# Kernel tuning notes

Hardware: AMD Instinct MI355X
Metric: run time of the kernel (lower is better)

## Reference

```python
import jax, jax.numpy as jnp
import numpy as np

B, IN, OUT, GD, TD, H, W, L = 16, 512, 256, 256, 256, 32, 32, 32
EPS_BN = 1e-5


def _conv2d(x, w, pad):
    return jax.lax.conv_general_dilated(
        x, w, window_strides=(1, 1), padding=[(pad, pad), (pad, pad)],
        dimension_numbers=("NCHW", "OIHW", "NCHW"))


def _up2(x):
    return jnp.repeat(jnp.repeat(x, 2, axis=2), 2, axis=3)


def _l2n(v):  # F.normalize(p=2, dim=1), eps=1e-12
    n = jnp.sqrt(jnp.sum(v * v, axis=1, keepdims=True))
    return v / jnp.maximum(n, 1e-12)


def _context(img_embs, words_embs, mask):
    i = _l2n(img_embs)            # [B, TD, P]
    wd = _l2n(words_embs)         # [B, TD, L]
    sim = jnp.einsum("bcp,bcl->bpl", i, wd)
    sim = jnp.where(mask[:, None, :], -jnp.inf, sim)
    attn = jax.nn.softmax(sim, axis=-1)
    return jnp.einsum("bpl,bcl->bcp", attn, wd)  # [B, TD, P]


def _bn(x, w, b):  # training-mode BatchNorm2d, biased variance
    m = jnp.mean(x, axis=(0, 2, 3), keepdims=True)
    v = jnp.var(x, axis=(0, 2, 3), keepdims=True)
    return (x - m) * jax.lax.rsqrt(v + EPS_BN) * w[None, :, None, None] + b[None, :, None, None]


def setup_inputs():
    key = jax.random.key(0)
    ks = jax.random.split(key, 16)
    s = 0.02
    COND = GD + TD
    return {
        "x": jax.random.normal(ks[0], (B, IN, H, W), jnp.float32),
        "global_cond": jax.random.normal(ks[1], (B, GD), jnp.float32),
        "words_embs": jax.random.normal(ks[2], (B, TD, L), jnp.float32),
        "mask": jax.random.randint(ks[3], (B, L), 0, 2).astype(bool),
        "w_img1": jax.random.normal(ks[4], (TD, IN), jnp.float32) * s,
        "w_img2": jax.random.normal(ks[5], (TD, OUT), jnp.float32) * s,
        "w_c1": jax.random.normal(ks[6], (OUT, IN, 3, 3), jnp.float32) * s,
        "w_c2": jax.random.normal(ks[7], (OUT, OUT, 3, 3), jnp.float32) * s,
        "bn1_w": jnp.ones((IN,), jnp.float32),
        "bn1_b": jnp.zeros((IN,), jnp.float32),
        "bn2_w": jnp.ones((OUT,), jnp.float32),
        "bn2_b": jnp.zeros((OUT,), jnp.float32),
        "w_g1": jax.random.normal(ks[8], (IN, COND), jnp.float32) * s,
        "b_g1": jnp.zeros((IN,), jnp.float32),
        "w_b1": jax.random.normal(ks[9], (IN, COND), jnp.float32) * s,
        "b_b1": jnp.zeros((IN,), jnp.float32),
        "w_g2": jax.random.normal(ks[10], (OUT, COND), jnp.float32) * s,
        "b_g2": jnp.zeros((OUT,), jnp.float32),
        "w_b2": jax.random.normal(ks[11], (OUT, COND), jnp.float32) * s,
        "b_b2": jnp.zeros((OUT,), jnp.float32),
        "w_sc": jax.random.normal(ks[12], (OUT, IN, 1, 1), jnp.float32) * s,
        "b_sc": jnp.zeros((OUT,), jnp.float32),
    }


def reference(x, global_cond, words_embs, mask,
              w_img1, w_img2, w_c1, w_c2,
              bn1_w, bn1_b, bn2_w, bn2_b,
              w_g1, b_g1, w_b1, b_b1,
              w_g2, b_g2, w_b2, b_b2,
              w_sc, b_sc):
    # ---- residual path, stage 1 ----
    img1 = jnp.einsum("tc,bcp->btp", w_img1, x.reshape(B, IN, H * W))
    ctx1 = _context(img1, words_embs, mask)                 # [B, TD, H*W]
    gc = jnp.broadcast_to(global_cond[:, :, None], (B, GD, H * W))
    cond1 = jnp.concatenate([gc, ctx1], axis=1)             # [B, GD+TD, H*W]
    gamma1 = jnp.einsum("oc,bcp->bop", w_g1, cond1) + b_g1[None, :, None]
    beta1 = jnp.einsum("oc,bcp->bop", w_b1, cond1) + b_b1[None, :, None]
    out = gamma1.reshape(B, IN, H, W) * _bn(x, bn1_w, bn1_b) + beta1.reshape(B, IN, H, W)
    out = jax.nn.relu(out)
    out = _up2(out)                                         # [B, IN, 2H, 2W]
    out = _conv2d(out, w_c1, 1)                             # [B, OUT, 2H, 2W]
    h2, w2 = 2 * H, 2 * W
    # ---- residual path, stage 2 ----
    img2 = jnp.einsum("tc,bcp->btp", w_img2, out.reshape(B, OUT, h2 * w2))
    ctx2 = _context(img2, words_embs, mask)                 # [B, TD, h2*w2]
    gc2 = jnp.broadcast_to(global_cond[:, :, None], (B, GD, h2 * w2))
    cond2 = jnp.concatenate([gc2, ctx2], axis=1)
    gamma2 = jnp.einsum("oc,bcp->bop", w_g2, cond2) + b_g2[None, :, None]
    beta2 = jnp.einsum("oc,bcp->bop", w_b2, cond2) + b_b2[None, :, None]
    out = gamma2.reshape(B, OUT, h2, w2) * _bn(out, bn2_w, bn2_b) + beta2.reshape(B, OUT, h2, w2)
    out = jax.nn.relu(out)
    out = _conv2d(out, w_c2, 1)
    # ---- shortcut ----
    sc = _conv2d(_up2(x), w_sc, 0) + b_sc[None, :, None, None]
    return out + sc
```

## Files before the change

### kernel.cpp

```cpp
#include <hip/hip_runtime.h>
#include <hip/hip_bf16.h>
#include <math.h>

#define NB 16
#define CIN1 512
#define COUT 256
#define GD 256
#define TD 256
#define LL 32
#define P1 1024
#define P2 4096
#define CONDC 512

typedef __attribute__((ext_vector_type(8))) short bf16x8;
typedef __attribute__((ext_vector_type(4))) float f32x4;
typedef unsigned short u16;

__device__ __forceinline__ u16 f2b(float f) {
  __hip_bfloat16 h = __float2bfloat16(f);
  return *(u16*)&h;
}
__device__ __forceinline__ float b2f(u16 v) {
  unsigned u = ((unsigned)v) << 16;
  float f;
  __builtin_memcpy(&f, &u, 4);
  return f;
}

__global__ void bn_stats_x_kernel(const float* __restrict__ x, float* __restrict__ mean,
                                  float* __restrict__ rstd, u16* __restrict__ xbf,
                                  int C, int HW) {
  int c = blockIdx.x, t = threadIdx.x;
  float s = 0.f, sq = 0.f;
  for (int b = 0; b < NB; ++b) {
    size_t base = ((size_t)b * C + c) * HW;
    for (int i = t; i < HW; i += 256) {
      float v = x[base + i];
      s += v; sq += v * v;
      xbf[base + i] = f2b(v);
    }
  }
  __shared__ float ss[256], sq2[256];
  ss[t] = s; sq2[t] = sq; __syncthreads();
  for (int o = 128; o > 0; o >>= 1) {
    if (t < o) { ss[t] += ss[t + o]; sq2[t] += sq2[t + o]; }
    __syncthreads();
  }
  if (t == 0) {
    float n = (float)NB * (float)HW;
    float m = ss[0] / n;
    float v = sq2[0] / n - m * m;
    mean[c] = m;
    rstd[c] = rsqrtf(v + 1e-5f);
  }
}

__global__ void bn_fin_kernel(const float* __restrict__ part, float* __restrict__ mean,
                              float* __restrict__ rstd) {
  int c = threadIdx.x;
  float s = 0.f, sq = 0.f;
  const float* ps = part + (size_t)c * 256;
  const float* pq = part + 65536 + (size_t)c * 256;
  for (int i = 0; i < 256; ++i) { s += ps[i]; sq += pq[i]; }
  float n = 16.f * 4096.f;
  float m = s / n;
  mean[c] = m;
  rstd[c] = rsqrtf(sq / n - m * m + 1e-5f);
}

__global__ void wdn_kernel(const float* __restrict__ we, float* __restrict__ wdn) {
  int b = blockIdx.x >> 5, l = blockIdx.x & 31;
  int t = threadIdx.x;
  const float* base = we + (size_t)b * TD * LL + l;
  float v[4]; float sq = 0.f;
#pragma unroll
  for (int k = 0; k < 4; ++k) { v[k] = base[(size_t)(t * 4 + k) * LL]; sq += v[k] * v[k]; }
#pragma unroll
  for (int o = 32; o > 0; o >>= 1) sq += __shfl_xor(sq, o);
  float r = 1.f / fmaxf(sqrtf(sq), 1e-12f);
  float* ob = wdn + (size_t)b * TD * LL + l;
#pragma unroll
  for (int k = 0; k < 4; ++k) ob[(size_t)(t * 4 + k) * LL] = v[k] * r;
}

__global__ __launch_bounds__(256) void attnctx_kernel(
    const u16* __restrict__ img, const float* __restrict__ wdn,
    const int* __restrict__ mask, u16* __restrict__ ctx, int P) {
  __shared__ u16 imgT[2][64 * 72];
  __shared__ u16 wdnT[32 * 264];
  __shared__ u16 wdnC[256 * 40];
  __shared__ u16 attnB[64 * 40];
  __shared__ float sqP[4][64];
  __shared__ float rnL[64];
  const int b = blockIdx.y, p0 = blockIdx.x * 64;
  const int tid = threadIdx.x;
  const int w = tid >> 6, lane = tid & 63;
  const int l15 = lane & 15, lg = lane >> 4;
  const u16* ib = img + (size_t)b * TD * P;
  const float* wb = wdn + (size_t)b * TD * LL;

  for (int i = tid; i < TD * LL; i += 256) {
    int t = i >> 5, l = i & 31;
    u16 v = f2b(wb[i]);
    wdnT[l * 264 + t] = v;
    wdnC[t * 40 + l] = v;
  }

  f32x4 s0 = {}, s1 = {};
  float ssq = 0.f;
  unsigned pk[8];
#pragma unroll
  for (int i = 0; i < 8; ++i) {
    int t = w * 16 + 2 * i;
    u16 h0 = ib[(size_t)t * P + p0 + lane];
    u16 h1 = ib[(size_t)(t + 1) * P + p0 + lane];
    float v0 = b2f(h0), v1 = b2f(h1);
    ssq += v0 * v0 + v1 * v1;
    pk[i] = (unsigned)h0 | ((unsigned)h1 << 16);
  }
#pragma unroll
  for (int i = 0; i < 8; ++i)
    *(unsigned*)(imgT[0] + lane * 72 + w * 16 + 2 * i) = pk[i];
  __syncthreads();

  for (int q = 0; q < 4; ++q) {
    const int cur = q & 1;
    if (q < 3) {
#pragma unroll
      for (int i = 0; i < 8; ++i) {
        int t = (q + 1) * 64 + w * 16 + 2 * i;
        u16 h0 = ib[(size_t)t * P + p0 + lane];
        u16 h1 = ib[(size_t)(t + 1) * P + p0 + lane];
        float v0 = b2f(h0), v1 = b2f(h1);
        ssq += v0 * v0 + v1 * v1;
        pk[i] = (unsigned)h0 | ((unsigned)h1 << 16);
      }
    }
#pragma unroll
    for (int ks = 0; ks < 2; ++ks) {
      bf16x8 a = *(const bf16x8*)(imgT[cur] + (w * 16 + l15) * 72 + ks * 32 + lg * 8);
      bf16x8 b0 = *(const bf16x8*)(wdnT + l15 * 264 + q * 64 + ks * 32 + lg * 8);
      bf16x8 b1 = *(const bf16x8*)(wdnT + (16 + l15) * 264 + q * 64 + ks * 32 + lg * 8);
      s0 = __builtin_amdgcn_mfma_f32_16x16x32_bf16(a, b0, s0, 0, 0, 0);
      s1 = __builtin_amdgcn_mfma_f32_16x16x32_bf16(a, b1, s1, 0, 0, 0);
    }
    if (q < 3) {
#pragma unroll
      for (int i = 0; i < 8; ++i)
        *(unsigned*)(imgT[cur ^ 1] + lane * 72 + w * 16 + 2 * i) = pk[i];
      __syncthreads();
    }
  }
  sqP[w][lane] = ssq;
  __syncthreads();
  if (tid < 64) {
    float s = sqP[0][tid] + sqP[1][tid] + sqP[2][tid] + sqP[3][tid];
    rnL[tid] = 1.f / fmaxf(sqrtf(s), 1e-12f);
  }
  __syncthreads();
  const bool m0 = mask[b * LL + l15] != 0;
  const bool m1 = mask[b * LL + 16 + l15] != 0;
#pragma unroll
  for (int k = 0; k < 4; ++k) {
    float rn = rnL[w * 16 + lg * 4 + k];
    float v0 = m0 ? -INFINITY : s0[k] * rn;
    float v1 = m1 ? -INFINITY : s1[k] * rn;
    float mx = fmaxf(v0, v1);
#pragma unroll
    for (int o = 1; o < 16; o <<= 1) mx = fmaxf(mx, __shfl_xor(mx, o));
    float e0 = expf(v0 - mx), e1 = expf(v1 - mx);
    float sm = e0 + e1;
#pragma unroll
    for (int o = 1; o < 16; o <<= 1) sm += __shfl_xor(sm, o);
    float inv = 1.f / sm;
    int px = w * 16 + lg * 4 + k;
    attnB[px * 40 + l15] = f2b(e0 * inv);
    attnB[px * 40 + 16 + l15] = f2b(e1 * inv);
  }
  __syncthreads();
  f32x4 acc[4][4] = {};
  bf16x8 bfr[4];
#pragma unroll
  for (int pt = 0; pt < 4; ++pt)
    bfr[pt] = *(const bf16x8*)(attnB + (pt * 16 + l15) * 40 + lg * 8);
#pragma unroll
  for (int cc = 0; cc < 4; ++cc) {
    bf16x8 a = *(const bf16x8*)(wdnC + ((w * 4 + cc) * 16 + l15) * 40 + lg * 8);
#pragma unroll
    for (int pt = 0; pt < 4; ++pt)
      acc[cc][pt] = __builtin_amdgcn_mfma_f32_16x16x32_bf16(a, bfr[pt], acc[cc][pt], 0, 0, 0);
  }
#pragma unroll
  for (int cc = 0; cc < 4; ++cc) {
#pragma unroll
    for (int pt = 0; pt < 4; ++pt) {
#pragma unroll
      for (int k = 0; k < 4; ++k) {
        int c = (w * 4 + cc) * 16 + lg * 4 + k;
        ctx[((size_t)b * TD + c) * P + p0 + pt * 16 + l15] = f2b(acc[cc][pt][k]);
      }
    }
  }
}

__global__ __launch_bounds__(256) void attnimg_kernel(
    const u16* __restrict__ W2p, const u16* __restrict__ xin,
    const float* __restrict__ wdn, const int* __restrict__ mask,
    u16* __restrict__ ctx, int P) {
  __shared__ u16 smem[(33792 + 16896) / 2];
  __shared__ float rnL[64];
  u16* imgT  = smem;
  u16* Xl    = smem + 16896;
  u16* wdnT  = smem + 16896;
  u16* wdnC  = smem;
  u16* attnB = smem + 10240;
  const int b = blockIdx.y, p0 = blockIdx.x * 64;
  const int tid = threadIdx.x;
  const int w = tid >> 6, lane = tid & 63;
  const int l15 = lane & 15, lg = lane >> 4;
  const u16* xb = xin + (size_t)b * COUT * P;
  const float* wb = wdn + (size_t)b * TD * LL;

  const int xr = tid >> 3, xcG = tid & 7;
  const int csw = xr ^ (((xcG >> 1) & 3) << 3);
  const u16* xsrc = xb + (size_t)xr * P + p0 + xcG * 8;
  u16 xst[8];
  {
    union { u16 u[8]; uint4 q; } xu;
    xu.q = *(const uint4*)xsrc;
#pragma unroll
    for (int i = 0; i < 8; ++i) xst[i] = xu.u[i];
  }
#pragma unroll
  for (int i = 0; i < 8; ++i)
    Xl[(xcG * 8 + i) * 40 + csw] = xst[i];
  __syncthreads();

  f32x4 acc[16];
#pragma unroll
  for (int tt = 0; tt < 16; ++tt) acc[tt] = (f32x4){0.f, 0.f, 0.f, 0.f};
  for (int c0b = 0; c0b < 8; ++c0b) {
    const int cur = c0b & 1;
    if (c0b + 1 < 8) {
      union { u16 u[8]; uint4 q; } xu;
      xu.q = *(const uint4*)(xsrc + (size_t)((c0b + 1) * 32) * P);
#pragma unroll
      for (int i = 0; i < 8; ++i) xst[i] = xu.u[i];
    }
    bf16x8 aA = *(const bf16x8*)(Xl + cur * 2560 + (w * 16 + l15) * 40 + ((lg ^ w) << 3));
#pragma unroll
    for (int tt = 0; tt < 16; ++tt) {
      bf16x8 bfr = *(const bf16x8*)(W2p + (((size_t)c0b * 16 + tt) * 64 + lane) * 8);
      acc[tt] = __builtin_amdgcn_mfma_f32_16x16x32_bf16(aA, bfr, acc[tt], 0, 0, 0);
    }
    if (c0b + 1 < 8) {
      const int nxt = cur ^ 1;
#pragma unroll
      for (int i = 0; i < 8; ++i)
        Xl[nxt * 2560 + (xcG * 8 + i) * 40 + csw] = xst[i];
      __syncthreads();
    }
  }
#pragma unroll
  for (int k = 0; k < 4; ++k) {
    float s = 0.f;
#pragma unroll
    for (int tt = 0; tt < 16; ++tt) s += acc[tt][k] * acc[tt][k];
#pragma unroll
    for (int o = 1; o < 16; o <<= 1) s += __shfl_xor(s, o);
    if (l15 == 0) rnL[w * 16 + lg * 4 + k] = 1.f / fmaxf(sqrtf(s), 1e-12f);
  }
#pragma unroll
  for (int tt = 0; tt < 16; ++tt)
#pragma unroll
    for (int k = 0; k < 4; ++k)
      imgT[(w * 16 + lg * 4 + k) * 264 + tt * 16 + l15] = f2b(acc[tt][k]);
  __syncthreads();

  for (int i = tid; i < TD * LL; i += 256) {
    int t = i >> 5, l = i & 31;
    wdnT[l * 264 + t] = f2b(wb[i]);
  }
  __syncthreads();
  f32x4 s0 = {}, s1 = {};
#pragma unroll
  for (int q = 0; q < 4; ++q) {
#pragma unroll
    for (int ks = 0; ks < 2; ++ks) {
      bf16x8 a = *(const bf16x8*)(imgT + (w * 16 + l15) * 264 + q * 64 + ks * 32 + lg * 8);
      bf16x8 b0 = *(const bf16x8*)(wdnT + l15 * 264 + q * 64 + ks * 32 + lg * 8);
      bf16x8 b1 = *(const bf16x8*)(wdnT + (16 + l15) * 264 + q * 64 + ks * 32 + lg * 8);
      s0 = __builtin_amdgcn_mfma_f32_16x16x32_bf16(a, b0, s0, 0, 0, 0);
      s1 = __builtin_amdgcn_mfma_f32_16x16x32_bf16(a, b1, s1, 0, 0, 0);
    }
  }
  const bool m0 = mask[b * LL + l15] != 0;
  const bool m1 = mask[b * LL + 16 + l15] != 0;
  float a0[4], a1[4];
#pragma unroll
  for (int k = 0; k < 4; ++k) {
    float rn = rnL[w * 16 + lg * 4 + k];
    float v0 = m0 ? -INFINITY : s0[k] * rn;
    float v1 = m1 ? -INFINITY : s1[k] * rn;
    float mx = fmaxf(v0, v1);
#pragma unroll
    for (int o = 1; o < 16; o <<= 1) mx = fmaxf(mx, __shfl_xor(mx, o));
    float e0 = expf(v0 - mx), e1 = expf(v1 - mx);
    float sm = e0 + e1;
#pragma unroll
    for (int o = 1; o < 16; o <<= 1) sm += __shfl_xor(sm, o);
    float inv = 1.f / sm;
    a0[k] = e0 * inv; a1[k] = e1 * inv;
  }
  __syncthreads();

  for (int i = tid; i < TD * LL; i += 256) {
    int t = i >> 5, l = i & 31;
    wdnC[t * 40 + l] = f2b(wb[i]);
  }
#pragma unroll
  for (int k = 0; k < 4; ++k) {
    int px = w * 16 + lg * 4 + k;
    attnB[px * 40 + l15] = f2b(a0[k]);
    attnB[px * 40 + 16 + l15] = f2b(a1[k]);
  }
  __syncthreads();
  f32x4 acc2[4][4] = {};
  bf16x8 bfr[4];
#pragma unroll
  for (int pt = 0; pt < 4; ++pt)
    bfr[pt] = *(const bf16x8*)(attnB + (pt * 16 + l15) * 40 + lg * 8);
#pragma unroll
  for (int cc = 0; cc < 4; ++cc) {
    bf16x8 a = *(const bf16x8*)(wdnC + ((w * 4 + cc) * 16 + l15) * 40 + lg * 8);
#pragma unroll
    for (int pt = 0; pt < 4; ++pt)
      acc2[cc][pt] = __builtin_amdgcn_mfma_f32_16x16x32_bf16(a, bfr[pt], acc2[cc][pt], 0, 0, 0);
  }
#pragma unroll
  for (int cc = 0; cc < 4; ++cc) {
#pragma unroll
    for (int pt = 0; pt < 4; ++pt) {
#pragma unroll
      for (int k = 0; k < 4; ++k) {
        int c = (w * 4 + cc) * 16 + lg * 4 + k;
        ctx[((size_t)b * TD + c) * P + p0 + pt * 16 + l15] = f2b(acc2[cc][pt][k]);
      }
    }
  }
}

template <bool XB, bool YB>
__global__ __launch_bounds__(256, 2) void gemm_mfma_kernel(
    const float* __restrict__ W, int ldw, int c_off,
    const void* __restrict__ Xv, const float* __restrict__ vec,
    void* __restrict__ Yv, int T, int C, int P) {
  __shared__ u16 Wl[2][128 * 44];
  __shared__ u16 Xl[2][128 * 40];
  const int b = blockIdx.z;
  const int t0 = blockIdx.y * 128, p0 = blockIdx.x * 128;
  const int tid = threadIdx.x;
  const int w = tid >> 6, lane = tid & 63;
  const int wo = w >> 1, wq = w & 1;
  const int l15 = lane & 15, lg = lane >> 4;
  const int wr = tid >> 1, wcH = tid & 1;
  const int xr = tid >> 3, xcG = tid & 7;
  const int csw = xr ^ ((xcG & 3) << 3);
  const float* wsrc = W + (size_t)(t0 + wr) * ldw + c_off + wcH * 16;
  const float* xsrc32 = XB ? nullptr : (const float*)Xv + (size_t)b * C * P + (size_t)xr * P + p0 + xcG * 16;
  const u16* xsrc16 = XB ? (const u16*)Xv + (size_t)b * C * P + (size_t)xr * P + p0 + xcG * 16 : nullptr;
  const int NK = C / 32;
  f32x4 acc[4][4] = {};
  float4 wreg[4];
  u16 xst[16];

#pragma unroll
  for (int j = 0; j < 4; ++j) wreg[j] = *(const float4*)(wsrc + j * 4);
  if (XB) {
    union { u16 u[16]; uint4 q[2]; } xu;
    xu.q[0] = *(const uint4*)(xsrc16);
    xu.q[1] = *(const uint4*)(xsrc16 + 8);
#pragma unroll
    for (int i = 0; i < 16; ++i) xst[i] = xu.u[i];
  } else {
#pragma unroll
    for (int j = 0; j < 4; ++j) {
      float4 v = *(const float4*)(xsrc32 + j * 4);
      xst[j * 4 + 0] = f2b(v.x); xst[j * 4 + 1] = f2b(v.y);
      xst[j * 4 + 2] = f2b(v.z); xst[j * 4 + 3] = f2b(v.w);
    }
  }
  {
    u16* dst = Wl[0] + wr * 44 + wcH * 16;
#pragma unroll
    for (int j = 0; j < 4; ++j)
      *(ushort4*)(dst + j * 4) = make_ushort4(f2b(wreg[j].x), f2b(wreg[j].y), f2b(wreg[j].z), f2b(wreg[j].w));
#pragma unroll
    for (int i = 0; i < 16; ++i)
      Xl[0][(xcG * 16 + i) * 40 + csw] = xst[i];
  }
  __syncthreads();

  for (int kb = 0; kb < NK; ++kb) {
    const int cur = kb & 1;
    if (kb + 1 < NK) {
      const int c0n = (kb + 1) * 32;
#pragma unroll
      for (int j = 0; j < 4; ++j) wreg[j] = *(const float4*)(wsrc + c0n + j * 4);
      if (XB) {
        union { u16 u[16]; uint4 q[2]; } xu;
        xu.q[0] = *(const uint4*)(xsrc16 + (size_t)c0n * P);
        xu.q[1] = *(const uint4*)(xsrc16 + (size_t)c0n * P + 8);
#pragma unroll
        for (int i = 0; i < 16; ++i) xst[i] = xu.u[i];
      } else {
#pragma unroll
        for (int j = 0; j < 4; ++j) {
          float4 v = *(const float4*)(xsrc32 + (size_t)c0n * P + j * 4);
          xst[j * 4 + 0] = f2b(v.x); xst[j * 4 + 1] = f2b(v.y);
          xst[j * 4 + 2] = f2b(v.z); xst[j * 4 + 3] = f2b(v.w);
        }
      }
    }
    bf16x8 a[4], bb[4];
#pragma unroll
    for (int rr = 0; rr < 4; ++rr)
      a[rr] = *(const bf16x8*)(Wl[cur] + (wo * 64 + rr * 16 + l15) * 44 + lg * 8);
#pragma unroll
    for (int ss = 0; ss < 4; ++ss)
      bb[ss] = *(const bf16x8*)(Xl[cur] + (wq * 64 + ss * 16 + l15) * 40 + ((lg ^ ss) << 3));
#pragma unroll
    for (int rr = 0; rr < 4; ++rr)
#pragma unroll
      for (int ss = 0; ss < 4; ++ss)
        acc[rr][ss] = __builtin_amdgcn_mfma_f32_16x16x32_bf16(a[rr], bb[ss], acc[rr][ss], 0, 0, 0);
    if (kb + 1 < NK) {
      const int nxt = cur ^ 1;
      u16* dst = Wl[nxt] + wr * 44 + wcH * 16;
#pragma unroll
      for (int j = 0; j < 4; ++j)
        *(ushort4*)(dst + j * 4) = make_ushort4(f2b(wreg[j].x), f2b(wreg[j].y), f2b(wreg[j].z), f2b(wreg[j].w));
#pragma unroll
      for (int i = 0; i < 16; ++i)
        Xl[nxt][(xcG * 16 + i) * 40 + csw] = xst[i];
      __syncthreads();
    }
  }
#pragma unroll
  for (int rr = 0; rr < 4; ++rr) {
    int tb = t0 + wo * 64 + rr * 16 + lg * 4;
#pragma unroll
    for (int ss = 0; ss < 4; ++ss) {
      int p = p0 + wq * 64 + ss * 16 + l15;
#pragma unroll
      for (int k = 0; k < 4; ++k) {
        int t = tb + k;
        float val = acc[rr][ss][k];
        if (vec) val += vec[(size_t)b * T + t];
        if (YB) ((u16*)Yv)[((size_t)b * T + t) * P + p] = f2b(val);
        else    ((float*)Yv)[((size_t)b * T + t) * P + p] = val;
      }
    }
  }
}

template <bool XINB>
__global__ __launch_bounds__(256, 2) void gbact_kernel(
    const float* __restrict__ Wg, const float* __restrict__ bg,
    const float* __restrict__ Wb, const float* __restrict__ bb_,
    const u16* __restrict__ ctx, const float* __restrict__ gcond,
    const void* __restrict__ xinv,
    const float* __restrict__ mean, const float* __restrict__ rstd,
    const float* __restrict__ bnw, const float* __restrict__ bnb,
    u16* __restrict__ outb, int C, int P) {
  __shared__ u16 shmem[2][16384];
  __shared__ float gvl[128], bvl[128];
  const int b = blockIdx.z, t0 = blockIdx.y * 128, p0 = blockIdx.x * 128;
  const int tid = threadIdx.x;
  const int w = tid >> 6, lane = tid & 63;
  const int wo = w >> 1, wq = w & 1;
  const int l15 = lane & 15, lg = lane >> 4;
  const int wr = tid >> 1, wcH = tid & 1;
  const int xr = tid >> 3, xcG = tid & 7;
  const int csw = xr ^ ((xcG & 3) << 3);
  const float* gsrc = Wg + (size_t)(t0 + wr) * CONDC + GD + wcH * 16;
  const float* bsrc = Wb + (size_t)(t0 + wr) * CONDC + GD + wcH * 16;
  const u16* xsrc = ctx + (size_t)b * TD * P + (size_t)xr * P + p0 + xcG * 16;
  const int NK = TD / 32;
  f32x4 accg[4][4] = {}, accb[4][4] = {};
  float4 greg[4], breg[4];
  u16 xst[16];

  {
    int t = tid & 127;
    const float* row = (tid < 128 ? Wg : Wb) + (size_t)(t0 + t) * CONDC;
    const float* gc = gcond + (size_t)b * GD;
    float s = 0.f;
    for (int c = 0; c < GD; c += 4) {
      float4 wv = *(const float4*)(row + c);
      float4 gv4 = *(const float4*)(gc + c);
      s += wv.x * gv4.x + wv.y * gv4.y + wv.z * gv4.z + wv.w * gv4.w;
    }
    s += (tid < 128 ? bg : bb_)[t0 + t];
    if (tid < 128) gvl[t] = s; else bvl[t] = s;
  }

#pragma unroll
  for (int j = 0; j < 4; ++j) {
    greg[j] = *(const float4*)(gsrc + j * 4);
    breg[j] = *(const float4*)(bsrc + j * 4);
  }
  {
    union { u16 u[16]; uint4 q[2]; } xu;
    xu.q[0] = *(const uint4*)(xsrc);
    xu.q[1] = *(const uint4*)(xsrc + 8);
#pragma unroll
    for (int i = 0; i < 16; ++i) xst[i] = xu.u[i];
  }
  {
    u16* dg = shmem[0] + wr * 44 + wcH * 16;
    u16* db = shmem[0] + 5632 + wr * 44 + wcH * 16;
    u16* xl = shmem[0] + 11264;
#pragma unroll
    for (int j = 0; j < 4; ++j) {
      *(ushort4*)(dg + j * 4) = make_ushort4(f2b(greg[j].x), f2b(greg[j].y), f2b(greg[j].z), f2b(greg[j].w));
      *(ushort4*)(db + j * 4) = make_ushort4(f2b(breg[j].x), f2b(breg[j].y), f2b(breg[j].z), f2b(breg[j].w));
    }
#pragma unroll
    for (int i = 0; i < 16; ++i)
      xl[(xcG * 16 + i) * 40 + csw] = xst[i];
  }
  __syncthreads();

  for (int kb = 0; kb < NK; ++kb) {
    const int cur = kb & 1;
    if (kb + 1 < NK) {
      const int c0n = (kb + 1) * 32;
#pragma unroll
      for (int j = 0; j < 4; ++j) {
        greg[j] = *(const float4*)(gsrc + c0n + j * 4);
        breg[j] = *(const float4*)(bsrc + c0n + j * 4);
      }
      union { u16 u[16]; uint4 q[2]; } xu;
      xu.q[0] = *(const uint4*)(xsrc + (size_t)c0n * P);
      xu.q[1] = *(const uint4*)(xsrc + (size_t)c0n * P + 8);
#pragma unroll
      for (int i = 0; i < 16; ++i) xst[i] = xu.u[i];
    }
    bf16x8 ag[4], ab[4], bb[4];
#pragma unroll
    for (int rr = 0; rr < 4; ++rr) {
      ag[rr] = *(const bf16x8*)(shmem[cur] + (wo * 64 + rr * 16 + l15) * 44 + lg * 8);
      ab[rr] = *(const bf16x8*)(shmem[cur] + 5632 + (wo * 64 + rr * 16 + l15) * 44 + lg * 8);
    }
#pragma unroll
    for (int ss = 0; ss < 4; ++ss)
      bb[ss] = *(const bf16x8*)(shmem[cur] + 11264 + (wq * 64 + ss * 16 + l15) * 40 + ((lg ^ ss) << 3));
#pragma unroll
    for (int rr = 0; rr < 4; ++rr)
#pragma unroll
      for (int ss = 0; ss < 4; ++ss) {
        accg[rr][ss] = __builtin_amdgcn_mfma_f32_16x16x32_bf16(ag[rr], bb[ss], accg[rr][ss], 0, 0, 0);
        accb[rr][ss] = __builtin_amdgcn_mfma_f32_16x16x32_bf16(ab[rr], bb[ss], accb[rr][ss], 0, 0, 0);
      }
    if (kb + 1 < NK) {
      const int nxt = cur ^ 1;
      u16* dg = shmem[nxt] + wr * 44 + wcH * 16;
      u16* db = shmem[nxt] + 5632 + wr * 44 + wcH * 16;
      u16* xl = shmem[nxt] + 11264;
#pragma unroll
      for (int j = 0; j < 4; ++j) {
        *(ushort4*)(dg + j * 4) = make_ushort4(f2b(greg[j].x), f2b(greg[j].y), f2b(greg[j].z), f2b(greg[j].w));
        *(ushort4*)(db + j * 4) = make_ushort4(f2b(breg[j].x), f2b(breg[j].y), f2b(breg[j].z), f2b(breg[j].w));
      }
#pragma unroll
      for (int i = 0; i < 16; ++i)
        xl[(xcG * 16 + i) * 40 + csw] = xst[i];
      __syncthreads();
    }
  }
  __syncthreads();
  u16* tbuf = &shmem[0][0];
#pragma unroll
  for (int rr = 0; rr < 4; ++rr) {
    float gv[4], bv[4], mm[4], rs[4], bB[4];
#pragma unroll
    for (int k = 0; k < 4; ++k) {
      int cl = wo * 64 + rr * 16 + lg * 4 + k;
      int c = t0 + cl;
      gv[k] = gvl[cl];
      bv[k] = bvl[cl];
      mm[k] = mean[c]; rs[k] = rstd[c] * bnw[c]; bB[k] = bnb[c];
    }
#pragma unroll
    for (int ss = 0; ss < 4; ++ss) {
#pragma unroll
      for (int k = 0; k < 4; ++k) {
        int cl = wo * 64 + rr * 16 + lg * 4 + k;
        int pl = wq * 64 + ss * 16 + l15;
        size_t xidx = ((size_t)b * C + t0 + cl) * P + p0 + pl;
        float xv = XINB ? b2f(((const u16*)xinv)[xidx]) : ((const float*)xinv)[xidx];
        float g = accg[rr][ss][k] + gv[k];
        float be = accb[rr][ss][k] + bv[k];
        float val = fmaxf(g * ((xv - mm[k]) * rs[k] + bB[k]) + be, 0.f);
        tbuf[pl * 136 + cl] = f2b(val);
      }
    }
  }
  __syncthreads();
  const int pr = tid >> 1, h = tid & 1;
#pragma unroll
  for (int j = 0; j < 8; ++j) {
    uint4 v = *(uint4*)(tbuf + pr * 136 + h * 64 + j * 8);
    *(uint4*)(outb + ((size_t)b * P + p0 + pr) * C + t0 + h * 64 + j * 8) = v;
  }
}

__global__ void pack3_kernel(const float* __restrict__ w1, u16* __restrict__ wp1,
                             const float* __restrict__ w2, u16* __restrict__ wp2,
                             const float* __restrict__ wi2, u16* __restrict__ w2p) {
  int lin = blockIdx.x * 256 + threadIdx.x;
  const int N1 = COUT * CIN1;
  const int N2 = COUT * COUT;
  if (lin < N1 + N2) {
    const float* w; u16* wp; int CIN;
    if (lin < N1) { w = w1; wp = wp1; CIN = CIN1; }
    else { lin -= N1; w = w2; wp = wp2; CIN = COUT; }
    int o = lin / CIN, c = lin - o * CIN;
    int c0blk = c >> 5, lg = (c >> 3) & 3, cc = c & 7;
    int ot = o >> 4, l15 = o & 15;
    int lane = lg * 16 + l15;
    size_t base = (((size_t)c0blk * (COUT >> 4) + ot) * 64 + lane) * 8 + cc;
    size_t posStride = (size_t)(CIN >> 5) * (COUT >> 4) * 512;
    const float* src = w + ((size_t)o * CIN + c) * 9;
#pragma unroll
    for (int pos = 0; pos < 9; ++pos)
      wp[pos * posStride + base] = f2b(src[pos]);
  } else {
    lin -= N1 + N2;
    if (lin >= COUT * COUT) return;
    int t = lin >> 8, c = lin & 255;
    int tt = t >> 4, l15 = t & 15;
    int c0b = c >> 5, lg = (c >> 3) & 3, cc = c & 7;
    w2p[(((size_t)c0b * 16 + tt) * 64 + lg * 16 + l15) * 8 + cc] = f2b(wi2[(size_t)t * COUT + c]);
  }
}

template <int CIN, bool UP, bool OUTB, bool STATS>
__global__ __launch_bounds__(512, 2) void conv_mfma_kernel(
    const u16* __restrict__ Wp, const u16* __restrict__ Xt,
    const u16* __restrict__ scs, const float* __restrict__ scb,
    void* __restrict__ Yv, float* __restrict__ part) {
  constexpr int S = UP ? 32 : 64;
  constexpr int NC0 = CIN >> 5;
  constexpr int NCH = 6 * 66 * 8;
  __shared__ u16 Xs[2][6 * 66 * 36];
  __shared__ float stats_ls[256], stats_lsq[256];
  const int b = blockIdx.z, pxT = blockIdx.x;
  const int tid = threadIdx.x;
  const int w = tid >> 6, lane = tid & 63;
  const int wo = w >> 2, wp_ = w & 3;
  const int l15 = lane & 15, lg = lane >> 4;
  const int Y0 = pxT * 4;
  const u16* Xb = Xt + (size_t)b * S * S * CIN;
  const size_t posStride = (size_t)NC0 * 16 * 512;
  f32x4 acc[8][4] = {};
  uint2 st[7];

  if (STATS && tid < 256) { stats_ls[tid] = 0.f; stats_lsq[tid] = 0.f; }

#pragma unroll
  for (int j = 0; j < 7; ++j) {
    int i = tid + j * 512;
    if (i < NCH) {
      int r = i / 528, rem = i - r * 528, col = rem >> 3, ch = rem & 7;
      int uy = Y0 - 1 + r, ux = col - 1;
      uint2 v = make_uint2(0u, 0u);
      if (uy >= 0 && uy < 64 && ux >= 0 && ux < 64) {
        int sy = UP ? (uy >> 1) : uy, sx = UP ? (ux >> 1) : ux;
        v = *(const uint2*)(Xb + ((size_t)sy * S + sx) * CIN + ch * 4);
      }
      st[j] = v;
    }
  }
#pragma unroll
  for (int j = 0; j < 7; ++j) {
    int i = tid + j * 512;
    if (i < NCH) {
      int r = i / 528, rem = i - r * 528, col = rem >> 3, ch = rem & 7;
      *(uint2*)(&Xs[0][(r * 66 + col) * 36 + ch * 4]) = st[j];
    }
  }
  __syncthreads();

  for (int c0b = 0; c0b < NC0; ++c0b) {
    const int cur = c0b & 1;
    if (c0b + 1 < NC0) {
      const int c0n = (c0b + 1) << 5;
#pragma unroll
      for (int j = 0; j < 7; ++j) {
        int i = tid + j * 512;
        if (i < NCH) {
          int r = i / 528, rem = i - r * 528, col = rem >> 3, ch = rem & 7;
          int uy = Y0 - 1 + r, ux = col - 1;
          uint2 v = make_uint2(0u, 0u);
          if (uy >= 0 && uy < 64 && ux >= 0 && ux < 64) {
            int sy = UP ? (uy >> 1) : uy, sx = UP ? (ux >> 1) : ux;
            v = *(const uint2*)(Xb + ((size_t)sy * S + sx) * CIN + c0n + ch * 4);
          }
          st[j] = v;
        }
      }
    }
    {
      const u16* wbB = Wp + ((size_t)c0b * 16 + wo * 8) * 512 + lane * 8;
      bf16x8 aC[8], aN[8];
#pragma unroll
      for (int rr = 0; rr < 8; ++rr)
        aC[rr] = *(const bf16x8*)(wbB + rr * 512);
#pragma unroll
      for (int pos = 0; pos < 9; ++pos) {
        const int ky = pos / 3, kx = pos - ky * 3;
        if (pos < 8) {
          const u16* wbn = wbB + (size_t)(pos + 1) * posStride;
#pragma unroll
          for (int rr = 0; rr < 8; ++rr)
            aN[rr] = *(const bf16x8*)(wbn + rr * 512);
        }
        const int rowb = ((wp_ + ky) * 66 + kx) * 36 + lg * 8;
#pragma unroll
        for (int ss = 0; ss < 4; ++ss) {
          int idx = rowb + (ss * 16 + l15) * 36;
          union { uint2 q[2]; bf16x8 v; } u;
          u.q[0] = *(const uint2*)(&Xs[cur][idx]);
          u.q[1] = *(const uint2*)(&Xs[cur][idx + 4]);
#pragma unroll
          for (int rr = 0; rr < 8; ++rr)
            acc[rr][ss] = __builtin_amdgcn_mfma_f32_16x16x32_bf16(aC[rr], u.v, acc[rr][ss], 0, 0, 0);
        }
#pragma unroll
        for (int rr = 0; rr < 8; ++rr) aC[rr] = aN[rr];
      }
    }
    if (c0b + 1 < NC0) {
#pragma unroll
      for (int j = 0; j < 7; ++j) {
        int i = tid + j * 512;
        if (i < NCH) {
          int r = i / 528, rem = i - r * 528, col = rem >> 3, ch = rem & 7;
          *(uint2*)(&Xs[cur ^ 1][(r * 66 + col) * 36 + ch * 4]) = st[j];
        }
      }
      __syncthreads();
    }
  }
  const int oBase = wo * 128 + lg * 4;
  const int pxBase = pxT * 256 + wp_ * 64 + l15;
  const int y = Y0 + wp_;
#pragma unroll
  for (int rr = 0; rr < 8; ++rr) {
#pragma unroll
    for (int ss = 0; ss < 4; ++ss) {
      int px = pxBase + ss * 16;
#pragma unroll
      for (int k = 0; k < 4; ++k) {
        int o = oBase + rr * 16 + k;
        float val = acc[rr][ss][k];
        if (scs) {
          int gx = px & 63;
          val += b2f(scs[((size_t)b * COUT + o) * P1 + (y >> 1) * 32 + (gx >> 1)]) + scb[o];
        }
        if (OUTB) ((u16*)Yv)[((size_t)b * COUT + o) * 4096 + px] = f2b(val);
        else      ((float*)Yv)[((size_t)b * COUT + o) * 4096 + px] = val;
      }
    }
  }
  if (STATS) {
#pragma unroll
    for (int rr = 0; rr < 8; ++rr) {
#pragma unroll
      for (int k = 0; k < 4; ++k) {
        float s = acc[rr][0][k] + acc[rr][1][k] + acc[rr][2][k] + acc[rr][3][k];
        float sq = acc[rr][0][k] * acc[rr][0][k] + acc[rr][1][k] * acc[rr][1][k] +
                   acc[rr][2][k] * acc[rr][2][k] + acc[rr][3][k] * acc[rr][3][k];
#pragma unroll
        for (int o = 1; o < 16; o <<= 1) { s += __shfl_xor(s, o); sq += __shfl_xor(sq, o); }
        if (l15 == 0) {
          int o_ = oBase + rr * 16 + k;
          atomicAdd(&stats_ls[o_], s);
          atomicAdd(&stats_lsq[o_], sq);
        }
      }
    }
    __syncthreads();
    if (tid < 256) {
      int blk = b * 16 + pxT;
      part[(size_t)tid * 256 + blk] = stats_ls[tid];
      part[65536 + (size_t)tid * 256 + blk] = stats_lsq[tid];
    }
  }
}

extern "C" void kernel_launch(void* const* d_in, const int* in_sizes, int n_in,
                              void* d_out, int out_size, void* d_ws, size_t ws_size,
                              hipStream_t stream) {
  const float* x      = (const float*)d_in[0];
  const float* gcond  = (const float*)d_in[1];
  const float* wemb   = (const float*)d_in[2];
  const int*   mask   = (const int*)d_in[3];
  const float* w_img1 = (const float*)d_in[4];
  const float* w_img2 = (const float*)d_in[5];
  const float* w_c1   = (const float*)d_in[6];
  const float* w_c2   = (const float*)d_in[7];
  const float* bn1_w  = (const float*)d_in[8];
  const float* bn1_b  = (const float*)d_in[9];
  const float* bn2_w  = (const float*)d_in[10];
  const float* bn2_b  = (const float*)d_in[11];
  const float* w_g1   = (const float*)d_in[12];
  const float* b_g1   = (const float*)d_in[13];
  const float* w_b1   = (const float*)d_in[14];
  const float* b_b1   = (const float*)d_in[15];
  const float* w_g2   = (const float*)d_in[16];
  const float* b_g2   = (const float*)d_in[17];
  const float* w_b2   = (const float*)d_in[18];
  const float* b_b2   = (const float*)d_in[19];
  const float* w_sc   = (const float*)d_in[20];
  const float* b_sc   = (const float*)d_in[21];
  float* out = (float*)d_out;
  float* ws = (float*)d_ws;

  const size_t MF = 16777216;
  float* A  = ws;
  float* Br = ws + MF;
  float* Cr = ws + 2 * MF;
  float* SM = ws + 3 * MF;
  float* wdn   = SM;
  float* mean1 = SM + 131072;
  float* rstd1 = mean1 + 512;
  float* mean2 = rstd1 + 512;
  float* rstd2 = mean2 + 256;
  float* part  = rstd2 + 256;
  float* wsp   = part + 131072;
  u16* Wp1 = (u16*)wsp;
  u16* Wp2 = (u16*)(wsp + 655360);
  u16* scs = (u16*)(wsp + 655360 + 294912);
  u16* W2p = (u16*)(wsp + 655360 + 294912 + 2097152);

  u16* img1   = (u16*)A;
  u16* ctx1   = (u16*)A + 4194304;
  u16* Xt1    = (u16*)A + 8388608;
  u16* xbf    = (u16*)A + 16777216;
  u16* conv1o = (u16*)Cr;
  u16* ctx2   = (u16*)A;
  u16* Xt2    = (u16*)Br;

  bn_stats_x_kernel<<<dim3(CIN1), dim3(256), 0, stream>>>(x, mean1, rstd1, xbf, CIN1, P1);
  wdn_kernel<<<dim3(NB * LL), dim3(64), 0, stream>>>(wemb, wdn);
  pack3_kernel<<<dim3((COUT * CIN1 + 2 * COUT * COUT + 255) / 256), dim3(256), 0, stream>>>(
      w_c1, Wp1, w_c2, Wp2, w_img2, W2p);
  gemm_mfma_kernel<true, true><<<dim3(P1 / 128, TD / 128, NB), dim3(256), 0, stream>>>(
      w_img1, CIN1, 0, xbf, nullptr, img1, TD, CIN1, P1);
  gemm_mfma_kernel<true, true><<<dim3(P1 / 128, COUT / 128, NB), dim3(256), 0, stream>>>(
      w_sc, CIN1, 0, xbf, nullptr, scs, COUT, CIN1, P1);
  attnctx_kernel<<<dim3(P1 / 64, NB), dim3(256), 0, stream>>>(img1, wdn, mask, ctx1, P1);
  gbact_kernel<true><<<dim3(P1 / 128, CIN1 / 128, NB), dim3(256), 0, stream>>>(
      w_g1, b_g1, w_b1, b_b1, ctx1, gcond, xbf, mean1, rstd1, bn1_w, bn1_b, Xt1, CIN1, P1);
  conv_mfma_kernel<CIN1, true, true, true><<<dim3(16, 1, NB), dim3(512), 0, stream>>>(
      Wp1, Xt1, nullptr, nullptr, conv1o, part);

  bn_fin_kernel<<<dim3(1), dim3(256), 0, stream>>>(part, mean2, rstd2);
  attnimg_kernel<<<dim3(P2 / 64, NB), dim3(256), 0, stream>>>(
      W2p, conv1o, wdn, mask, ctx2, P2);
  gbact_kernel<true><<<dim3(P2 / 128, COUT / 128, NB), dim3(256), 0, stream>>>(
      w_g2, b_g2, w_b2, b_b2, ctx2, gcond, conv1o, mean2, rstd2, bn2_w, bn2_b, Xt2, COUT, P2);
  conv_mfma_kernel<COUT, false, false, false><<<dim3(16, 1, NB), dim3(512), 0, stream>>>(
      Wp2, Xt2, scs, b_sc, out, nullptr);
}
```

Measured before the change: 458.1 us.

## Merge prelude kernels and fuse img1/shortcut GEMMs sharing the X tile

Three small setup kernels (BN stats with the bf16 cast of x, word-embedding normalisation, weight packing) are merged into one launch by splitting work on block index. The two 1x1 GEMMs that both read the bf16 x (w_img1 and w_sc) become one kernel. It loads each X tile into LDS once and keeps two sets of accumulators. This cuts launch count and duplicate X reads. In exchange, the fused GEMM doubles accumulator registers and LDS per block, which may lower occupancy, and the grid is half as large.

```diff
diff --git a/kernel.cpp b/kernel.cpp
--- a/kernel.cpp
+++ b/kernel.cpp
@@ -27,31 +27,77 @@
   return f;
 }
 
-__global__ void bn_stats_x_kernel(const float* __restrict__ x, float* __restrict__ mean,
-                                  float* __restrict__ rstd, u16* __restrict__ xbf,
-                                  int C, int HW) {
-  int c = blockIdx.x, t = threadIdx.x;
-  float s = 0.f, sq = 0.f;
-  for (int b = 0; b < NB; ++b) {
-    size_t base = ((size_t)b * C + c) * HW;
-    for (int i = t; i < HW; i += 256) {
-      float v = x[base + i];
-      s += v; sq += v * v;
-      xbf[base + i] = f2b(v);
-    }
-  }
-  __shared__ float ss[256], sq2[256];
-  ss[t] = s; sq2[t] = sq; __syncthreads();
-  for (int o = 128; o > 0; o >>= 1) {
-    if (t < o) { ss[t] += ss[t + o]; sq2[t] += sq2[t + o]; }
-    __syncthreads();
-  }
-  if (t == 0) {
-    float n = (float)NB * (float)HW;
-    float m = ss[0] / n;
-    float v = sq2[0] / n - m * m;
-    mean[c] = m;
-    rstd[c] = rsqrtf(v + 1e-5f);
+__global__ void prelude_kernel(const float* __restrict__ x, float* __restrict__ mean,
+                               float* __restrict__ rstd, u16* __restrict__ xbf,
+                               const float* __restrict__ we, float* __restrict__ wdn,
+                               const float* __restrict__ w1, u16* __restrict__ wp1,
+                               const float* __restrict__ w2, u16* __restrict__ wp2,
+                               const float* __restrict__ wi2, u16* __restrict__ w2p) {
+  const int bid = blockIdx.x;
+  if (bid < CIN1) {
+    int c = bid, t = threadIdx.x;
+    float s = 0.f, sq = 0.f;
+    for (int b = 0; b < NB; ++b) {
+      size_t base = ((size_t)b * CIN1 + c) * P1;
+      for (int i = t; i < P1; i += 256) {
+        float v = x[base + i];
+        s += v; sq += v * v;
+        xbf[base + i] = f2b(v);
+      }
+    }
+    __shared__ float ss[256], sq2[256];
+    ss[t] = s; sq2[t] = sq; __syncthreads();
+    for (int o = 128; o > 0; o >>= 1) {
+      if (t < o) { ss[t] += ss[t + o]; sq2[t] += sq2[t + o]; }
+      __syncthreads();
+    }
+    if (t == 0) {
+      float n = (float)NB * (float)P1;
+      float m = ss[0] / n;
+      float v = sq2[0] / n - m * m;
+      mean[c] = m;
+      rstd[c] = rsqrtf(v + 1e-5f);
+    }
+  } else if (bid < CIN1 + 128) {
+    int g = (bid - CIN1) * 4 + (threadIdx.x >> 6);
+    int b = g >> 5, l = g & 31;
+    int t = threadIdx.x & 63;
+    const float* base = we + (size_t)b * TD * LL + l;
+    float v[4]; float sq = 0.f;
+#pragma unroll
+    for (int k = 0; k < 4; ++k) { v[k] = base[(size_t)(t * 4 + k) * LL]; sq += v[k] * v[k]; }
+#pragma unroll
+    for (int o = 32; o > 0; o >>= 1) sq += __shfl_xor(sq, o);
+    float r = 1.f / fmaxf(sqrtf(sq), 1e-12f);
+    float* ob = wdn + (size_t)b * TD * LL + l;
+#pragma unroll
+    for (int k = 0; k < 4; ++k) ob[(size_t)(t * 4 + k) * LL] = v[k] * r;
+  } else {
+    int lin = (bid - CIN1 - 128) * 256 + threadIdx.x;
+    const int N1 = COUT * CIN1;
+    const int N2 = COUT * COUT;
+    if (lin < N1 + N2) {
+      const float* w; u16* wp; int CIN;
+      if (lin < N1) { w = w1; wp = wp1; CIN = CIN1; }
+      else { lin -= N1; w = w2; wp = wp2; CIN = COUT; }
+      int o = lin / CIN, c = lin - o * CIN;
+      int c0blk = c >> 5, lg = (c >> 3) & 3, cc = c & 7;
+      int ot = o >> 4, l15 = o & 15;
+      int lane = lg * 16 + l15;
+      size_t base = (((size_t)c0blk * (COUT >> 4) + ot) * 64 + lane) * 8 + cc;
+      size_t posStride = (size_t)(CIN >> 5) * (COUT >> 4) * 512;
+      const float* src = w + ((size_t)o * CIN + c) * 9;
+#pragma unroll
+      for (int pos = 0; pos < 9; ++pos)
+        wp[pos * posStride + base] = f2b(src[pos]);
+    } else {
+      lin -= N1 + N2;
+      if (lin >= COUT * COUT) return;
+      int t = lin >> 8, c = lin & 255;
+      int tt = t >> 4, l15 = t & 15;
+      int c0b = c >> 5, lg = (c >> 3) & 3, cc = c & 7;
+      w2p[(((size_t)c0b * 16 + tt) * 64 + lg * 16 + l15) * 8 + cc] = f2b(wi2[(size_t)t * COUT + c]);
+    }
   }
 }
 
@@ -66,21 +112,6 @@
   float m = s / n;
   mean[c] = m;
   rstd[c] = rsqrtf(sq / n - m * m + 1e-5f);
-}
-
-__global__ void wdn_kernel(const float* __restrict__ we, float* __restrict__ wdn) {
-  int b = blockIdx.x >> 5, l = blockIdx.x & 31;
-  int t = threadIdx.x;
-  const float* base = we + (size_t)b * TD * LL + l;
-  float v[4]; float sq = 0.f;
-#pragma unroll
-  for (int k = 0; k < 4; ++k) { v[k] = base[(size_t)(t * 4 + k) * LL]; sq += v[k] * v[k]; }
-#pragma unroll
-  for (int o = 32; o > 0; o >>= 1) sq += __shfl_xor(sq, o);
-  float r = 1.f / fmaxf(sqrtf(sq), 1e-12f);
-  float* ob = wdn + (size_t)b * TD * LL + l;
-#pragma unroll
-  for (int k = 0; k < 4; ++k) ob[(size_t)(t * 4 + k) * LL] = v[k] * r;
 }
 
 __global__ __launch_bounds__(256) void attnctx_kernel(
@@ -350,15 +381,12 @@
   }
 }
 
-template <bool XB, bool YB>
-__global__ __launch_bounds__(256, 2) void gemm_mfma_kernel(
-    const float* __restrict__ W, int ldw, int c_off,
-    const void* __restrict__ Xv, const float* __restrict__ vec,
-    void* __restrict__ Yv, int T, int C, int P) {
-  __shared__ u16 Wl[2][128 * 44];
-  __shared__ u16 Xl[2][128 * 40];
-  const int b = blockIdx.z;
-  const int t0 = blockIdx.y * 128, p0 = blockIdx.x * 128;
+__global__ __launch_bounds__(256, 2) void gemm2_mfma_kernel(
+    const float* __restrict__ W1, const float* __restrict__ W2,
+    const u16* __restrict__ X, u16* __restrict__ Y1, u16* __restrict__ Y2,
+    int C, int P) {
+  __shared__ u16 shmem[2][16384];
+  const int b = blockIdx.z, t0 = blockIdx.y * 128, p0 = blockIdx.x * 128;
   const int tid = threadIdx.x;
   const int w = tid >> 6, lane = tid & 63;
   const int wo = w >> 1, wq = w & 1;
@@ -366,38 +394,38 @@
   const int wr = tid >> 1, wcH = tid & 1;
   const int xr = tid >> 3, xcG = tid & 7;
   const int csw = xr ^ ((xcG & 3) << 3);
-  const float* wsrc = W + (size_t)(t0 + wr) * ldw + c_off + wcH * 16;
-  const float* xsrc32 = XB ? nullptr : (const float*)Xv + (size_t)b * C * P + (size_t)xr * P + p0 + xcG * 16;
-  const u16* xsrc16 = XB ? (const u16*)Xv + (size_t)b * C * P + (size_t)xr * P + p0 + xcG * 16 : nullptr;
+  const float* s1src = W1 + (size_t)(t0 + wr) * C + wcH * 16;
+  const float* s2src = W2 + (size_t)(t0 + wr) * C + wcH * 16;
+  const u16* xsrc = X + (size_t)b * C * P + (size_t)xr * P + p0 + xcG * 16;
   const int NK = C / 32;
-  f32x4 acc[4][4] = {};
-  float4 wreg[4];
+  f32x4 acc1[4][4] = {}, acc2[4][4] = {};
+  float4 w1reg[4], w2reg[4];
   u16 xst[16];
 
 #pragma unroll
-  for (int j = 0; j < 4; ++j) wreg[j] = *(const float4*)(wsrc + j * 4);
-  if (XB) {
+  for (int j = 0; j < 4; ++j) {
+    w1reg[j] = *(const float4*)(s1src + j * 4);
+    w2reg[j] = *(const float4*)(s2src + j * 4);
+  }
+  {
     union { u16 u[16]; uint4 q[2]; } xu;
-    xu.q[0] = *(const uint4*)(xsrc16);
-    xu.q[1] = *(const uint4*)(xsrc16 + 8);
+    xu.q[0] = *(const uint4*)(xsrc);
+    xu.q[1] = *(const uint4*)(xsrc + 8);
 #pragma unroll
     for (int i = 0; i < 16; ++i) xst[i] = xu.u[i];
-  } else {
+  }
+  {
+    u16* d1 = shmem[0] + wr * 44 + wcH * 16;
+    u16* d2 = shmem[0] + 5632 + wr * 44 + wcH * 16;
+    u16* xl = shmem[0] + 11264;
 #pragma unroll
     for (int j = 0; j < 4; ++j) {
-      float4 v = *(const float4*)(xsrc32 + j * 4);
-      xst[j * 4 + 0] = f2b(v.x); xst[j * 4 + 1] = f2b(v.y);
-      xst[j * 4 + 2] = f2b(v.z); xst[j * 4 + 3] = f2b(v.w);
-    }
-  }
-  {
-    u16* dst = Wl[0] + wr * 44 + wcH * 16;
-#pragma unroll
-    for (int j = 0; j < 4; ++j)
-      *(ushort4*)(dst + j * 4) = make_ushort4(f2b(wreg[j].x), f2b(wreg[j].y), f2b(wreg[j].z), f2b(wreg[j].w));
+      *(ushort4*)(d1 + j * 4) = make_ushort4(f2b(w1reg[j].x), f2b(w1reg[j].y), f2b(w1reg[j].z), f2b(w1reg[j].w));
+      *(ushort4*)(d2 + j * 4) = make_ushort4(f2b(w2reg[j].x), f2b(w2reg[j].y), f2b(w2reg[j].z), f2b(w2reg[j].w));
+    }
 #pragma unroll
     for (int i = 0; i < 16; ++i)
-      Xl[0][(xcG * 16 + i) * 40 + csw] = xst[i];
+      xl[(xcG * 16 + i) * 40 + csw] = xst[i];
   }
   __syncthreads();
 
@@ -406,43 +434,45 @@
     if (kb + 1 < NK) {
       const int c0n = (kb + 1) * 32;
 #pragma unroll
-      for (int j = 0; j < 4; ++j) wreg[j] = *(const float4*)(wsrc + c0n + j * 4);
-      if (XB) {
-        union { u16 u[16]; uint4 q[2]; } xu;
-        xu.q[0] = *(const uint4*)(xsrc16 + (size_t)c0n * P);
-        xu.q[1] = *(const uint4*)(xsrc16 + (size_t)c0n * P + 8);
-#pragma unroll
-        for (int i = 0; i < 16; ++i) xst[i] = xu.u[i];
-      } else {
-#pragma unroll
-        for (int j = 0; j < 4; ++j) {
-          float4 v = *(const float4*)(xsrc32 + (size_t)c0n * P + j * 4);
-          xst[j * 4 + 0] = f2b(v.x); xst[j * 4 + 1] = f2b(v.y);
-          xst[j * 4 + 2] = f2b(v.z); xst[j * 4 + 3] = f2b(v.w);
-        }
-      }
-    }
-    bf16x8 a[4], bb[4];
+      for (int j = 0; j < 4; ++j) {
+        w1reg[j] = *(const float4*)(s1src + c0n + j * 4);
+        w2reg[j] = *(const float4*)(s2src + c0n + j * 4);
+      }
+      union { u16 u[16]; uint4 q[2]; } xu;
+      xu.q[0] = *(const uint4*)(xsrc + (size_t)c0n * P);
+      xu.q[1] = *(const uint4*)(xsrc + (size_t)c0n * P + 8);
+#pragma unroll
+      for (int i = 0; i < 16; ++i) xst[i] = xu.u[i];
+    }
+    bf16x8 a1[4], a2[4], bb[4];
+#pragma unroll
+    for (int rr = 0; rr < 4; ++rr) {
+      a1[rr] = *(const bf16x8*)(shmem[cur] + (wo * 64 + rr * 16 + l15) * 44 + lg * 8);
+      a2[rr] = *(const bf16x8*)(shmem[cur] + 5632 + (wo * 64 + rr * 16 + l15) * 44 + lg * 8);
+    }
+#pragma unroll
+    for (int ss = 0; ss < 4; ++ss)
+      bb[ss] = *(const bf16x8*)(shmem[cur] + 11264 + (wq * 64 + ss * 16 + l15) * 40 + ((lg ^ ss) << 3));
 #pragma unroll
     for (int rr = 0; rr < 4; ++rr)
-      a[rr] = *(const bf16x8*)(Wl[cur] + (wo * 64 + rr * 16 + l15) * 44 + lg * 8);
-#pragma unroll
-    for (int ss = 0; ss < 4; ++ss)
-      bb[ss] = *(const bf16x8*)(Xl[cur] + (wq * 64 + ss * 16 + l15) * 40 + ((lg ^ ss) << 3));
-#pragma unroll
-    for (int rr = 0; rr < 4; ++rr)
-#pragma unroll
-      for (int ss = 0; ss < 4; ++ss)
-        acc[rr][ss] = __builtin_amdgcn_mfma_f32_16x16x32_bf16(a[rr], bb[ss], acc[rr][ss], 0, 0, 0);
+#pragma unroll
+      for (int ss = 0; ss < 4; ++ss) {
+        acc1[rr][ss] = __builtin_amdgcn_mfma_f32_16x16x32_bf16(a1[rr], bb[ss], acc1[rr][ss], 0, 0, 0);
+        acc2[rr][ss] = __builtin_amdgcn_mfma_f32_16x16x32_bf16(a2[rr], bb[ss], acc2[rr][ss], 0, 0, 0);
+      }
     if (kb + 1 < NK) {
       const int nxt = cur ^ 1;
-      u16* dst = Wl[nxt] + wr * 44 + wcH * 16;
-#pragma unroll
-      for (int j = 0; j < 4; ++j)
-        *(ushort4*)(dst + j * 4) = make_ushort4(f2b(wreg[j].x), f2b(wreg[j].y), f2b(wreg[j].z), f2b(wreg[j].w));
+      u16* d1 = shmem[nxt] + wr * 44 + wcH * 16;
+      u16* d2 = shmem[nxt] + 5632 + wr * 44 + wcH * 16;
+      u16* xl = shmem[nxt] + 11264;
+#pragma unroll
+      for (int j = 0; j < 4; ++j) {
+        *(ushort4*)(d1 + j * 4) = make_ushort4(f2b(w1reg[j].x), f2b(w1reg[j].y), f2b(w1reg[j].z), f2b(w1reg[j].w));
+        *(ushort4*)(d2 + j * 4) = make_ushort4(f2b(w2reg[j].x), f2b(w2reg[j].y), f2b(w2reg[j].z), f2b(w2reg[j].w));
+      }
 #pragma unroll
       for (int i = 0; i < 16; ++i)
-        Xl[nxt][(xcG * 16 + i) * 40 + csw] = xst[i];
+        xl[(xcG * 16 + i) * 40 + csw] = xst[i];
       __syncthreads();
     }
   }
@@ -455,10 +485,8 @@
 #pragma unroll
       for (int k = 0; k < 4; ++k) {
         int t = tb + k;
-        float val = acc[rr][ss][k];
-        if (vec) val += vec[(size_t)b * T + t];
-        if (YB) ((u16*)Yv)[((size_t)b * T + t) * P + p] = f2b(val);
-        else    ((float*)Yv)[((size_t)b * T + t) * P + p] = val;
+        Y1[((size_t)b * TD + t) * P + p] = f2b(acc1[rr][ss][k]);
+        Y2[((size_t)b * COUT + t) * P + p] = f2b(acc2[rr][ss][k]);
       }
     }
   }
@@ -613,36 +641,6 @@
   for (int j = 0; j < 8; ++j) {
     uint4 v = *(uint4*)(tbuf + pr * 136 + h * 64 + j * 8);
     *(uint4*)(outb + ((size_t)b * P + p0 + pr) * C + t0 + h * 64 + j * 8) = v;
-  }
-}
-
-__global__ void pack3_kernel(const float* __restrict__ w1, u16* __restrict__ wp1,
-                             const float* __restrict__ w2, u16* __restrict__ wp2,
-                             const float* __restrict__ wi2, u16* __restrict__ w2p) {
-  int lin = blockIdx.x * 256 + threadIdx.x;
-  const int N1 = COUT * CIN1;
-  const int N2 = COUT * COUT;
-  if (lin < N1 + N2) {
-    const float* w; u16* wp; int CIN;
-    if (lin < N1) { w = w1; wp = wp1; CIN = CIN1; }
-    else { lin -= N1; w = w2; wp = wp2; CIN = COUT; }
-    int o = lin / CIN, c = lin - o * CIN;
-    int c0blk = c >> 5, lg = (c >> 3) & 3, cc = c & 7;
-    int ot = o >> 4, l15 = o & 15;
-    int lane = lg * 16 + l15;
-    size_t base = (((size_t)c0blk * (COUT >> 4) + ot) * 64 + lane) * 8 + cc;
-    size_t posStride = (size_t)(CIN >> 5) * (COUT >> 4) * 512;
-    const float* src = w + ((size_t)o * CIN + c) * 9;
-#pragma unroll
-    for (int pos = 0; pos < 9; ++pos)
-      wp[pos * posStride + base] = f2b(src[pos]);
-  } else {
-    lin -= N1 + N2;
-    if (lin >= COUT * COUT) return;
-    int t = lin >> 8, c = lin & 255;
-    int tt = t >> 4, l15 = t & 15;
-    int c0b = c >> 5, lg = (c >> 3) & 3, cc = c & 7;
-    w2p[(((size_t)c0b * 16 + tt) * 64 + lg * 16 + l15) * 8 + cc] = f2b(wi2[(size_t)t * COUT + c]);
   }
 }
 
@@ -854,14 +852,10 @@
   u16* ctx2   = (u16*)A;
   u16* Xt2    = (u16*)Br;
 
-  bn_stats_x_kernel<<<dim3(CIN1), dim3(256), 0, stream>>>(x, mean1, rstd1, xbf, CIN1, P1);
-  wdn_kernel<<<dim3(NB * LL), dim3(64), 0, stream>>>(wemb, wdn);
-  pack3_kernel<<<dim3((COUT * CIN1 + 2 * COUT * COUT + 255) / 256), dim3(256), 0, stream>>>(
-      w_c1, Wp1, w_c2, Wp2, w_img2, W2p);
-  gemm_mfma_kernel<true, true><<<dim3(P1 / 128, TD / 128, NB), dim3(256), 0, stream>>>(
-      w_img1, CIN1, 0, xbf, nullptr, img1, TD, CIN1, P1);
-  gemm_mfma_kernel<true, true><<<dim3(P1 / 128, COUT / 128, NB), dim3(256), 0, stream>>>(
-      w_sc, CIN1, 0, xbf, nullptr, scs, COUT, CIN1, P1);
+  prelude_kernel<<<dim3(CIN1 + 128 + 1024), dim3(256), 0, stream>>>(
+      x, mean1, rstd1, xbf, wemb, wdn, w_c1, Wp1, w_c2, Wp2, w_img2, W2p);
+  gemm2_mfma_kernel<<<dim3(P1 / 128, 2, NB), dim3(256), 0, stream>>>(
+      w_img1, w_sc, xbf, img1, scs, CIN1, P1);
   attnctx_kernel<<<dim3(P1 / 64, NB), dim3(256), 0, stream>>>(img1, wdn, mask, ctx1, P1);
   gbact_kernel<true><<<dim3(P1 / 128, CIN1 / 128, NB), dim3(256), 0, stream>>>(
       w_g1, b_g1, w_b1, b_b1, ctx1, gcond, xbf, mean1, rstd1, bn1_w, bn1_b, Xt1, CIN1, P1);
```

Result: faster. 448.1 us (-2.2%).
